# Performance work log

Hardware: AMD Instinct MI355X
Metric: run time of the kernel (lower is better)

The kernel has to match this reference:

```python
import jax, jax.numpy as jnp
import numpy as np

N_HEAD = 16
D_HEAD = 64
D_HIDN = 1024
B, S = 2, 2048
MASK_FILL = -1e9


def setup_inputs() -> dict:
    key = jax.random.key(0)
    ks = jax.random.split(key, 8)
    scale = 1.0 / np.sqrt(D_HIDN)
    return {
        "Q": jax.random.normal(ks[0], (B, S, D_HIDN), dtype=jnp.float32),
        "K": jax.random.normal(ks[1], (B, S, D_HIDN), dtype=jnp.float32),
        "V": jax.random.normal(ks[2], (B, S, D_HIDN), dtype=jnp.float32),
        "attn_mask": jnp.zeros((B, S, S), dtype=jnp.bool_),
        "Wq": jax.random.normal(ks[3], (D_HIDN, N_HEAD * D_HEAD), dtype=jnp.float32) * scale,
        "bq": jnp.zeros((N_HEAD * D_HEAD,), dtype=jnp.float32),
        "Wk": jax.random.normal(ks[4], (D_HIDN, N_HEAD * D_HEAD), dtype=jnp.float32) * scale,
        "bk": jnp.zeros((N_HEAD * D_HEAD,), dtype=jnp.float32),
        "Wv": jax.random.normal(ks[5], (D_HIDN, N_HEAD * D_HEAD), dtype=jnp.float32) * scale,
        "bv": jnp.zeros((N_HEAD * D_HEAD,), dtype=jnp.float32),
        "Wo": jax.random.normal(ks[6], (N_HEAD * D_HEAD, D_HIDN), dtype=jnp.float32) * scale,
        "bo": jnp.zeros((D_HIDN,), dtype=jnp.float32),
    }


def reference(Q, K, V, attn_mask, Wq, bq, Wk, bk, Wv, bv, Wo, bo):
    b, s, _ = Q.shape
    # projections -> [B, H, S, d_head]
    def split_heads(x):
        return x.reshape(b, -1, N_HEAD, D_HEAD).transpose(0, 2, 1, 3)
    q = split_heads(Q @ Wq + bq)
    k = split_heads(K @ Wk + bk)
    v = split_heads(V @ Wv + bv)
    # scaled dot-product attention with masked_fill(-1e9)
    scores = jnp.einsum("bhqd,bhkd->bhqk", q, k) / jnp.sqrt(jnp.float32(D_HEAD))
    scores = jnp.where(attn_mask[:, None, :, :], MASK_FILL, scores)
    attn_prob = jax.nn.softmax(scores, axis=-1)  # [B,H,S,S]
    context = jnp.einsum("bhqk,bhkd->bhqd", attn_prob, v)
    context = context.transpose(0, 2, 1, 3).reshape(b, s, N_HEAD * D_HEAD)
    output = context @ Wo + bo  # dropout is identity at eval
    return output, attn_prob
```

## Files before the change

kernel.cpp:

```cpp
#include <hip/hip_runtime.h>

typedef _Float16 f16;
typedef _Float16 f16x8 __attribute__((ext_vector_type(8)));
typedef _Float16 f16x4v __attribute__((ext_vector_type(4)));
typedef float f32x4 __attribute__((ext_vector_type(4)));

#define B_   2
#define S_   2048
#define H_   16
#define DH   64
#define DM   1024
#define BS_  (B_ * S_)

#if __has_builtin(__builtin_amdgcn_exp2f)
#define EXP2(x) __builtin_amdgcn_exp2f(x)
#else
#define EXP2(x) exp2f(x)
#endif

#define SCHED_FENCE() __builtin_amdgcn_sched_barrier(0)

__device__ __forceinline__ void gload16(const void* g, void* l) {
  __builtin_amdgcn_global_load_lds((const __attribute__((address_space(1))) unsigned int*)g,
                                   (__attribute__((address_space(3))) unsigned int*)l, 16, 0, 0);
}

__global__ __launch_bounds__(256) void prep(const float* __restrict__ Q, const float* __restrict__ K,
                                            const float* __restrict__ V,
                                            f16* __restrict__ Xq, f16* __restrict__ Xk, f16* __restrict__ Xv,
                                            const float* __restrict__ w0, const float* __restrict__ w1,
                                            const float* __restrict__ w2, const float* __restrict__ w3,
                                            f16* __restrict__ t0, f16* __restrict__ t1,
                                            f16* __restrict__ t2, f16* __restrict__ t3,
                                            const unsigned char* __restrict__ mask,
                                            unsigned* __restrict__ mtab) {
  int bid = blockIdx.x;
  int tid = threadIdx.x;
  if (bid < 6144) {
    int t = bid >> 11;
    const float* in = t == 0 ? Q : (t == 1 ? K : V);
    f16* out = t == 0 ? Xq : (t == 1 ? Xk : Xv);
    int i = ((bid & 2047) * 256 + tid) * 8;
    float4 x = *(const float4*)(in + i);
    float4 y = *(const float4*)(in + i + 4);
    f16x8 o;
    o[0] = (f16)x.x; o[1] = (f16)x.y; o[2] = (f16)x.z; o[3] = (f16)x.w;
    o[4] = (f16)y.x; o[5] = (f16)y.y; o[6] = (f16)y.z; o[7] = (f16)y.w;
    *(f16x8*)(out + i) = o;
  } else if (bid < 7168) {
    __shared__ float t[64][65];
    int w = bid - 6144;
    int z = w >> 8, rr = w & 255;
    const float* wsrc = z == 0 ? w0 : (z == 1 ? w1 : (z == 2 ? w2 : w3));
    f16* wt = z == 0 ? t0 : (z == 1 ? t1 : (z == 2 ? t2 : t3));
    int r0 = (rr >> 4) * 64, c0 = (rr & 15) * 64;
    int tr = tid >> 2, seg = tid & 3;
#pragma unroll
    for (int jj = 0; jj < 4; ++jj) {
      float4 v = *(const float4*)(wsrc + (size_t)(r0 + tr) * DM + c0 + seg * 16 + jj * 4);
      t[tr][seg * 16 + jj * 4 + 0] = v.x;
      t[tr][seg * 16 + jj * 4 + 1] = v.y;
      t[tr][seg * 16 + jj * 4 + 2] = v.z;
      t[tr][seg * 16 + jj * 4 + 3] = v.w;
    }
    __syncthreads();
#pragma unroll
    for (int jj = 0; jj < 2; ++jj) {
      f16x8 o;
#pragma unroll
      for (int e = 0; e < 8; ++e) o[e] = (f16)t[seg * 16 + jj * 8 + e][tr];
      *(f16x8*)(wt + (size_t)(c0 + tr) * DM + r0 + seg * 16 + jj * 8) = o;
    }
  } else {
    __shared__ unsigned mbits;
    if (tid == 0) mbits = 0;
    __syncthreads();
    int mb_id = bid - 7168;
    int b = mb_id >> 4, qt = mb_id & 15;
    int row = qt * 128 + (tid >> 1), halfsel = tid & 1;
    const unsigned char* mrow = mask + (size_t)b * S_ * S_ + (size_t)row * S_ + halfsel * 1024;
    unsigned bits = 0;
#pragma unroll
    for (int c = 0; c < 16; ++c) {
      uint4 a0 = *(const uint4*)(mrow + c * 64);
      uint4 a1 = *(const uint4*)(mrow + c * 64 + 16);
      uint4 a2 = *(const uint4*)(mrow + c * 64 + 32);
      uint4 a3 = *(const uint4*)(mrow + c * 64 + 48);
      unsigned z = (a0.x|a0.y|a0.z|a0.w) | (a1.x|a1.y|a1.z|a1.w) |
                   (a2.x|a2.y|a2.z|a2.w) | (a3.x|a3.y|a3.z|a3.w);
      bits |= (z != 0 ? 1u : 0u) << (halfsel * 16 + c);
    }
    if (bits) atomicOr(&mbits, bits);
    __syncthreads();
    if (tid == 0) mtab[mb_id] = mbits;
  }
}

__device__ __forceinline__ void gemm_core(const f16* __restrict__ A,
                                          const f16* __restrict__ Bt,
                                          int m0, int n0,
                                          char (&As)[2][16384], char (&Bs)[2][16384],
                                          f32x4 (&acc)[4][2]) {
  const int tid = threadIdx.x;
  const int lane = tid & 63, wid = tid >> 6;
  const int wr = wid >> 2, wc = wid & 3;
  const int l15 = lane & 15, l4 = lane >> 4;
#pragma unroll
  for (int mi = 0; mi < 4; ++mi)
#pragma unroll
    for (int ni = 0; ni < 2; ++ni) { acc[mi][ni][0]=0.f; acc[mi][ni][1]=0.f; acc[mi][ni][2]=0.f; acc[mi][ni][3]=0.f; }

  auto stage = [&](int buf, int kt) {
#pragma unroll
    for (int j = 0; j < 2; ++j) {
      int L = j * 512 + tid;
      int row = L >> 3, seg = L & 7;
      int so = (seg ^ (row & 7)) << 4;
      gload16((const char*)A + ((size_t)(m0 + row) * DM + kt) * 2 + so,
              As[buf] + j * 8192 + wid * 1024);
      gload16((const char*)Bt + ((size_t)(n0 + row) * DM + kt) * 2 + so,
              Bs[buf] + j * 8192 + wid * 1024);
    }
  };

  stage(0, 0);
  __syncthreads();
  for (int t = 0; t < 16; ++t) {
    int cur = t & 1;
    if (t < 15) stage(cur ^ 1, (t + 1) * 64);
#pragma unroll
    for (int kk = 0; kk < 2; ++kk) {
      f16x8 af[4], bf[2];
#pragma unroll
      for (int mi = 0; mi < 4; ++mi) {
        int row = wr * 64 + mi * 16 + l15;
        af[mi] = *(const f16x8*)(As[cur] + row * 128 + ((kk * 64 + l4 * 16) ^ ((row & 7) << 4)));
      }
#pragma unroll
      for (int ni = 0; ni < 2; ++ni) {
        int row = wc * 32 + ni * 16 + l15;
        bf[ni] = *(const f16x8*)(Bs[cur] + row * 128 + ((kk * 64 + l4 * 16) ^ ((row & 7) << 4)));
      }
#pragma unroll
      for (int mi = 0; mi < 4; ++mi)
#pragma unroll
        for (int ni = 0; ni < 2; ++ni)
          acc[mi][ni] = __builtin_amdgcn_mfma_f32_16x16x32_f16(af[mi], bf[ni], acc[mi][ni], 0, 0, 0);
    }
    __syncthreads();
  }
}

struct GemmPtrs { const f16* A; const f16* Bt; const float* bias; f16* outh; };

__global__ __launch_bounds__(512, 4) void gemm_proj(GemmPtrs p0, GemmPtrs p1, GemmPtrs p2,
                                                    f16* __restrict__ vout) {
  __shared__ __attribute__((aligned(16))) char As[2][16384];
  __shared__ __attribute__((aligned(16))) char Bs[2][16384];
  int lin = (blockIdx.z * 8 + blockIdx.y) * 32 + blockIdx.x;
  int swz = (lin & 7) * 96 + (lin >> 3);
  int z = swz >> 8, r = swz & 255;
  int m0 = (r >> 3) * 128, n0 = (r & 7) * 128;
  GemmPtrs g = z == 0 ? p0 : (z == 1 ? p1 : p2);

  f32x4 acc[4][2];
  gemm_core(g.A, g.Bt, m0, n0, As, Bs, acc);

  const int tid = threadIdx.x;
  const int lane = tid & 63, wid = tid >> 6;
  const int wr = wid >> 2, wc = wid & 3;
  const int l15 = lane & 15, l4 = lane >> 4;

  if (z != 2) {
#pragma unroll
    for (int mi = 0; mi < 4; ++mi)
#pragma unroll
      for (int ni = 0; ni < 2; ++ni) {
        int gcol = n0 + wc * 32 + ni * 16 + l15;
        float bv = g.bias[gcol];
#pragma unroll
        for (int rr = 0; rr < 4; ++rr) {
          int grow = m0 + wr * 64 + mi * 16 + l4 * 4 + rr;
          int b = grow >> 11, s = grow & 2047, h = gcol >> 6, d = gcol & 63;
          g.outh[(size_t)((b * H_ + h) * S_ + s) * DH + d] = (f16)(acc[mi][ni][rr] + bv);
        }
      }
  } else {
    f16* T2 = (f16*)&As[0][0];
    int b = m0 >> 11, s0 = m0 & 2047;
#pragma unroll
    for (int hh = 0; hh < 2; ++hh) {
      if ((wc >> 1) == hh) {
        int dl = (wc & 1) * 32;
#pragma unroll
        for (int mi = 0; mi < 4; ++mi)
#pragma unroll
          for (int ni = 0; ni < 2; ++ni) {
            int d = dl + ni * 16 + l15;
            int sl = wr * 64 + mi * 16 + l4 * 4;
            float bv = g.bias[n0 + hh * 64 + d];
            f16x4v pv;
            pv[0] = (f16)(acc[mi][ni][0] + bv);
            pv[1] = (f16)(acc[mi][ni][1] + bv);
            pv[2] = (f16)(acc[mi][ni][2] + bv);
            pv[3] = (f16)(acc[mi][ni][3] + bv);
            *(f16x4v*)(T2 + d * 136 + sl) = pv;
          }
      }
      __syncthreads();
      {
        int d = tid >> 3, sq = tid & 7;
        int head = (n0 >> 6) + hh;
        const f16* src = T2 + d * 136 + sq * 16;
        f16* dst = vout + ((size_t)((b * H_ + head) * DH + d)) * S_ + s0 + sq * 16;
        *(f16x8*)(dst)     = *(const f16x8*)(src);
        *(f16x8*)(dst + 8) = *(const f16x8*)(src + 8);
      }
      if (hh == 0) __syncthreads();
    }
  }
}

__global__ __launch_bounds__(512, 2) void gemm_out(const f16* __restrict__ A,
                                                   const f16* __restrict__ Bt,
                                                   const float* __restrict__ bias,
                                                   float* __restrict__ outf) {
  __shared__ __attribute__((aligned(16))) char As[2][16384];
  __shared__ __attribute__((aligned(16))) char Bs[2][16384];
  int lin = blockIdx.y * 32 + blockIdx.x;
  int swz = (lin & 7) * 32 + (lin >> 3);
  int m0 = (swz >> 3) * 128, n0 = (swz & 7) * 128;

  f32x4 acc[4][2];
  gemm_core(A, Bt, m0, n0, As, Bs, acc);

  const int tid = threadIdx.x;
  const int lane = tid & 63, wid = tid >> 6;
  const int wr = wid >> 2, wc = wid & 3;
  const int l15 = lane & 15, l4 = lane >> 4;
#pragma unroll
  for (int mi = 0; mi < 4; ++mi)
#pragma unroll
    for (int ni = 0; ni < 2; ++ni) {
      int gcol = n0 + wc * 32 + ni * 16 + l15;
      float bv = bias[gcol];
#pragma unroll
      for (int rr = 0; rr < 4; ++rr) {
        int grow = m0 + wr * 64 + mi * 16 + l4 * 4 + rr;
        outf[(size_t)grow * DM + gcol] = acc[mi][ni][rr] + bv;
      }
    }
}

__global__ __launch_bounds__(512, 4) void attn_kernel(const f16* __restrict__ q,
                                                      const f16* __restrict__ k,
                                                      const f16* __restrict__ vt,
                                                      const unsigned char* __restrict__ mask,
                                                      const unsigned* __restrict__ mtab,
                                                      float* __restrict__ pout,
                                                      f16* __restrict__ ctxh) {
  __shared__ __attribute__((aligned(16))) char KV[4][8192];
  __shared__ __attribute__((aligned(16))) float P32[8][16][68];
  const int tid = threadIdx.x;
  const int lane = tid & 63, wid = tid >> 6;
  const int l15 = lane & 15, l4 = lane >> 4;

  int lin = blockIdx.y * 16 + blockIdx.x;
  int swz = (lin & 7) * 64 + (lin >> 3);
  const int bx = swz & 15, bh = swz >> 4;
  const int b = bh >> 4, h = bh & 15;
  const int q0w = bx * 128 + wid * 16;

  const f16* qb = q + (size_t)bh * S_ * DH;
  const char* kbc = (const char*)(k + (size_t)bh * S_ * DH);
  const char* vtbc = (const char*)(vt + (size_t)bh * DH * S_);
  const unsigned char* mb = mask + (size_t)b * S_ * S_;
  float* pb = pout + (size_t)bh * S_ * S_;

  const int srow = tid >> 3, sseg = tid & 7;
  const int soff = (sseg ^ (srow & 7)) << 4;

  auto stageK = [&](int buf, int t) {
    gload16(kbc + (size_t)(t * 64 + srow) * 128 + soff, KV[buf] + wid * 1024);
  };
  auto stageV = [&](int buf, int t) {
    gload16(vtbc + (size_t)srow * (S_ * 2) + (size_t)(t * 64) * 2 + soff, KV[buf] + wid * 1024);
  };

  const unsigned mmask = mtab[b * 16 + bx];

  const f16 qs = (f16)0.18033688f;
  f16x8 aq[2];
#pragma unroll
  for (int hh = 0; hh < 2; ++hh) {
    f16x8 v = *(const f16x8*)(qb + (size_t)(q0w + l15) * DH + hh * 32 + l4 * 8);
#pragma unroll
    for (int j = 0; j < 8; ++j) v[j] = v[j] * qs;
    aq[hh] = v;
  }
  SCHED_FENCE();

  float sm[4] = {0.f, 0.f, 0.f, 0.f};

  stageK(0, 0);
  stageK(1, 1);
  for (int p = 0; p < 16; ++p) {
    asm volatile("s_waitcnt vmcnt(0)" ::: "memory");
    __builtin_amdgcn_s_barrier();
    SCHED_FENCE();
    if (p < 15) { stageK((2 * p + 2) & 3, 2 * p + 2); stageK((2 * p + 3) & 3, 2 * p + 3); }
    SCHED_FENCE();
#pragma unroll
    for (int u = 0; u < 2; ++u) {
      const int t = 2 * p + u;
      const char* Kb = KV[t & 3];
      const int kt = t * 64;
      const int anym = (mmask >> t) & 1;
#pragma unroll
      for (int f = 0; f < 4; ++f) {
        int krow = f * 16 + l15;
        f16x8 bk0 = *(const f16x8*)(Kb + krow * 128 + ((l4 * 16) ^ ((krow & 7) << 4)));
        f16x8 bk1 = *(const f16x8*)(Kb + krow * 128 + ((64 + l4 * 16) ^ ((krow & 7) << 4)));
        f32x4 s; s[0]=0.f; s[1]=0.f; s[2]=0.f; s[3]=0.f;
        __builtin_amdgcn_s_setprio(1);
        s = __builtin_amdgcn_mfma_f32_16x16x32_f16(aq[0], bk0, s, 0, 0, 0);
        s = __builtin_amdgcn_mfma_f32_16x16x32_f16(aq[1], bk1, s, 0, 0, 0);
        __builtin_amdgcn_s_setprio(0);
#pragma unroll
        for (int rr = 0; rr < 4; ++rr) {
          float sv = s[rr];
          if (anym) sv = mb[(size_t)(q0w + l4 * 4 + rr) * S_ + kt + f * 16 + l15] ? -1e9f : sv;
          sm[rr] += EXP2(sv);
        }
      }
    }
  }
#pragma unroll
  for (int d = 1; d < 16; d <<= 1)
#pragma unroll
    for (int rr = 0; rr < 4; ++rr) sm[rr] += __shfl_xor(sm[rr], d);
  float inv[4];
#pragma unroll
  for (int rr = 0; rr < 4; ++rr) inv[rr] = 1.0f / sm[rr];

  f32x4 ctx[4];
#pragma unroll
  for (int dc = 0; dc < 4; ++dc) { ctx[dc][0]=0.f; ctx[dc][1]=0.f; ctx[dc][2]=0.f; ctx[dc][3]=0.f; }

  __builtin_amdgcn_s_barrier();
  stageK(0, 0);
  stageV(2, 0);
  __syncthreads();
  for (int t = 0; t < 32; ++t) {
    const int cur = t & 1;
    const int kt = t * 64;
    if (t < 31) { stageK(cur ^ 1, t + 1); stageV(2 + (cur ^ 1), t + 1); }
    SCHED_FENCE();
    const int anym = (mmask >> t) & 1;

#pragma unroll
    for (int f = 0; f < 4; ++f) {
      int krow = f * 16 + l15;
      f16x8 bk0 = *(const f16x8*)(KV[cur] + krow * 128 + ((l4 * 16) ^ ((krow & 7) << 4)));
      f16x8 bk1 = *(const f16x8*)(KV[cur] + krow * 128 + ((64 + l4 * 16) ^ ((krow & 7) << 4)));
      f32x4 s; s[0]=0.f; s[1]=0.f; s[2]=0.f; s[3]=0.f;
      __builtin_amdgcn_s_setprio(1);
      s = __builtin_amdgcn_mfma_f32_16x16x32_f16(aq[0], bk0, s, 0, 0, 0);
      s = __builtin_amdgcn_mfma_f32_16x16x32_f16(aq[1], bk1, s, 0, 0, 0);
      __builtin_amdgcn_s_setprio(0);
#pragma unroll
      for (int rr = 0; rr < 4; ++rr) {
        float sv = s[rr];
        if (anym) sv = mb[(size_t)(q0w + l4 * 4 + rr) * S_ + kt + f * 16 + l15] ? -1e9f : sv;
        float p = EXP2(sv) * inv[rr];
        P32[wid][l4 * 4 + rr][f * 16 + l15] = p;
      }
    }
#pragma unroll
    for (int j = 0; j < 4; ++j) {
      int row = j * 4 + l4;
      f32x4 v = *(const f32x4*)&P32[wid][row][l15 * 4];
      __builtin_nontemporal_store(v, (f32x4*)(pb + (size_t)(q0w + row) * S_ + kt + l15 * 4));
    }
#pragma unroll
    for (int kk = 0; kk < 2; ++kk) {
      f32x4 x = *(const f32x4*)&P32[wid][l15][kk * 32 + l4 * 8];
      f32x4 y = *(const f32x4*)&P32[wid][l15][kk * 32 + l4 * 8 + 4];
      f16x8 pa;
      pa[0] = (f16)x[0]; pa[1] = (f16)x[1]; pa[2] = (f16)x[2]; pa[3] = (f16)x[3];
      pa[4] = (f16)y[0]; pa[5] = (f16)y[1]; pa[6] = (f16)y[2]; pa[7] = (f16)y[3];
      f16x8 bv0, bv1, bv2, bv3;
      {
        int vr0 = 0 * 16 + l15, vr1 = 1 * 16 + l15, vr2 = 2 * 16 + l15, vr3 = 3 * 16 + l15;
        bv0 = *(const f16x8*)(KV[2 + cur] + vr0 * 128 + ((kk * 64 + l4 * 16) ^ ((vr0 & 7) << 4)));
        bv1 = *(const f16x8*)(KV[2 + cur] + vr1 * 128 + ((kk * 64 + l4 * 16) ^ ((vr1 & 7) << 4)));
        bv2 = *(const f16x8*)(KV[2 + cur] + vr2 * 128 + ((kk * 64 + l4 * 16) ^ ((vr2 & 7) << 4)));
        bv3 = *(const f16x8*)(KV[2 + cur] + vr3 * 128 + ((kk * 64 + l4 * 16) ^ ((vr3 & 7) << 4)));
      }
      __builtin_amdgcn_s_setprio(1);
      ctx[0] = __builtin_amdgcn_mfma_f32_16x16x32_f16(pa, bv0, ctx[0], 0, 0, 0);
      ctx[1] = __builtin_amdgcn_mfma_f32_16x16x32_f16(pa, bv1, ctx[1], 0, 0, 0);
      ctx[2] = __builtin_amdgcn_mfma_f32_16x16x32_f16(pa, bv2, ctx[2], 0, 0, 0);
      ctx[3] = __builtin_amdgcn_mfma_f32_16x16x32_f16(pa, bv3, ctx[3], 0, 0, 0);
      __builtin_amdgcn_s_setprio(0);
    }

    if (t < 31) {
      asm volatile("s_waitcnt vmcnt(4)" ::: "memory");
      __builtin_amdgcn_s_barrier();
      SCHED_FENCE();
    }
  }

  {
    f16* cst = (f16*)&P32[wid][0][0];
#pragma unroll
    for (int dc = 0; dc < 4; ++dc)
#pragma unroll
      for (int rr = 0; rr < 4; ++rr)
        cst[(l4 * 4 + rr) * 72 + dc * 16 + l15] = (f16)ctx[dc][rr];
#pragma unroll
    for (int j = 0; j < 4; ++j) {
      int row = j * 4 + l4;
      f16x4v v = *(const f16x4v*)(cst + row * 72 + l15 * 4);
      *(f16x4v*)(ctxh + (size_t)(b * S_ + q0w + row) * DM + h * DH + l15 * 4) = v;
    }
  }
}

extern "C" void kernel_launch(void* const* d_in, const int* in_sizes, int n_in,
                              void* d_out, int out_size, void* d_ws, size_t ws_size,
                              hipStream_t stream) {
  (void)in_sizes; (void)n_in; (void)out_size; (void)ws_size;
  const float* Q  = (const float*)d_in[0];
  const float* K  = (const float*)d_in[1];
  const float* V  = (const float*)d_in[2];
  const unsigned char* mask = (const unsigned char*)d_in[3];
  const float* Wq = (const float*)d_in[4];
  const float* bq = (const float*)d_in[5];
  const float* Wk = (const float*)d_in[6];
  const float* bk = (const float*)d_in[7];
  const float* Wv = (const float*)d_in[8];
  const float* bv = (const float*)d_in[9];
  const float* Wo = (const float*)d_in[10];
  const float* bo = (const float*)d_in[11];

  f16* ws = (f16*)d_ws;
  f16* Xq  = ws;
  f16* Xk  = Xq + 4194304;
  f16* Xv  = Xk + 4194304;
  f16* Wqt = Xv + 4194304;
  f16* Wkt = Wqt + 1048576;
  f16* Wvt = Wkt + 1048576;
  f16* Wot = Wvt + 1048576;
  f16* qh  = Wot + 1048576;
  f16* kh  = qh + 4194304;
  f16* vth = kh + 4194304;
  unsigned* mtab = (unsigned*)(vth + 4194304);
  f16* ctx = Xq;

  float* out0 = (float*)d_out;
  float* pout = out0 + (size_t)BS_ * DM;

  prep<<<dim3(7200), dim3(256), 0, stream>>>(Q, K, V, Xq, Xk, Xv,
                                             Wq, Wk, Wv, Wo, Wqt, Wkt, Wvt, Wot,
                                             mask, mtab);

  GemmPtrs pq{Xq, Wqt, bq, qh};
  GemmPtrs pk{Xk, Wkt, bk, kh};
  GemmPtrs pv{Xv, Wvt, bv, nullptr};
  gemm_proj<<<dim3(32, 8, 3), dim3(512), 0, stream>>>(pq, pk, pv, vth);

  attn_kernel<<<dim3(16, 32), dim3(512), 0, stream>>>(qh, kh, vth, mask, mtab, pout, ctx);

  gemm_out<<<dim3(32, 8), dim3(512), 0, stream>>>(ctx, Wot, bo, out0);
}
```

Measured before the change: 228.1 us.

## Fuse fp32-to-fp16 activation conversion into projection GEMM A-tile loading

Drops the separate conversion of Q/K/V to fp16 from the prep kernel. The projection GEMM now loads fp32 A tiles straight into registers, converts them, and writes them into swizzled LDS after the MFMA step, overlapping with compute. This removes a full write and re-read of 24MB of fp16 activations. In exchange the A loads now go through registers, which raises register pressure in a kernel launched with a 4-blocks occupancy bound, and A traffic into the GEMM doubles because fp32 is read.

```diff
diff --git a/kernel.cpp b/kernel.cpp
--- a/kernel.cpp
+++ b/kernel.cpp
@@ -25,10 +25,7 @@
                                    (__attribute__((address_space(3))) unsigned int*)l, 16, 0, 0);
 }
 
-__global__ __launch_bounds__(256) void prep(const float* __restrict__ Q, const float* __restrict__ K,
-                                            const float* __restrict__ V,
-                                            f16* __restrict__ Xq, f16* __restrict__ Xk, f16* __restrict__ Xv,
-                                            const float* __restrict__ w0, const float* __restrict__ w1,
+__global__ __launch_bounds__(256) void prep(const float* __restrict__ w0, const float* __restrict__ w1,
                                             const float* __restrict__ w2, const float* __restrict__ w3,
                                             f16* __restrict__ t0, f16* __restrict__ t1,
                                             f16* __restrict__ t2, f16* __restrict__ t3,
@@ -36,21 +33,9 @@
                                             unsigned* __restrict__ mtab) {
   int bid = blockIdx.x;
   int tid = threadIdx.x;
-  if (bid < 6144) {
-    int t = bid >> 11;
-    const float* in = t == 0 ? Q : (t == 1 ? K : V);
-    f16* out = t == 0 ? Xq : (t == 1 ? Xk : Xv);
-    int i = ((bid & 2047) * 256 + tid) * 8;
-    float4 x = *(const float4*)(in + i);
-    float4 y = *(const float4*)(in + i + 4);
-    f16x8 o;
-    o[0] = (f16)x.x; o[1] = (f16)x.y; o[2] = (f16)x.z; o[3] = (f16)x.w;
-    o[4] = (f16)y.x; o[5] = (f16)y.y; o[6] = (f16)y.z; o[7] = (f16)y.w;
-    *(f16x8*)(out + i) = o;
-  } else if (bid < 7168) {
+  if (bid < 1024) {
     __shared__ float t[64][65];
-    int w = bid - 6144;
-    int z = w >> 8, rr = w & 255;
+    int z = bid >> 8, rr = bid & 255;
     const float* wsrc = z == 0 ? w0 : (z == 1 ? w1 : (z == 2 ? w2 : w3));
     f16* wt = z == 0 ? t0 : (z == 1 ? t1 : (z == 2 ? t2 : t3));
     int r0 = (rr >> 4) * 64, c0 = (rr & 15) * 64;
@@ -75,7 +60,7 @@
     __shared__ unsigned mbits;
     if (tid == 0) mbits = 0;
     __syncthreads();
-    int mb_id = bid - 7168;
+    int mb_id = bid - 1024;
     int b = mb_id >> 4, qt = mb_id & 15;
     int row = qt * 128 + (tid >> 1), halfsel = tid & 1;
     const unsigned char* mrow = mask + (size_t)b * S_ * S_ + (size_t)row * S_ + halfsel * 1024;
@@ -96,7 +81,8 @@
   }
 }
 
-__device__ __forceinline__ void gemm_core(const f16* __restrict__ A,
+template <bool A32>
+__device__ __forceinline__ void gemm_core(const void* __restrict__ Ap,
                                           const f16* __restrict__ Bt,
                                           int m0, int n0,
                                           char (&As)[2][16384], char (&Bs)[2][16384],
@@ -110,24 +96,76 @@
 #pragma unroll
     for (int ni = 0; ni < 2; ++ni) { acc[mi][ni][0]=0.f; acc[mi][ni][1]=0.f; acc[mi][ni][2]=0.f; acc[mi][ni][3]=0.f; }
 
-  auto stage = [&](int buf, int kt) {
+  const int arow = tid >> 2, aquad = tid & 3;
+  const float* Af = (const float*)Ap;
+  const f16* Ah = (const f16*)Ap;
+
+  f32x4 areg[4];
+  auto issueA = [&](int kt) {
+    if (A32) {
+#pragma unroll
+      for (int u = 0; u < 4; ++u)
+        areg[u] = *(const f32x4*)(Af + (size_t)(m0 + arow) * DM + kt + aquad * 16 + u * 4);
+    } else {
+#pragma unroll
+      for (int j = 0; j < 2; ++j) {
+        int L = j * 512 + tid;
+        int row = L >> 3, seg = L & 7;
+        int so = (seg ^ (row & 7)) << 4;
+        gload16((const char*)Ah + ((size_t)(m0 + row) * DM + 0) * 2 + (size_t)kt * 2 + so,
+                As[0] + j * 8192 + wid * 1024);
+      }
+    }
+  };
+  (void)issueA;
+
+  auto stageB = [&](int buf, int kt) {
 #pragma unroll
     for (int j = 0; j < 2; ++j) {
       int L = j * 512 + tid;
       int row = L >> 3, seg = L & 7;
       int so = (seg ^ (row & 7)) << 4;
-      gload16((const char*)A + ((size_t)(m0 + row) * DM + kt) * 2 + so,
-              As[buf] + j * 8192 + wid * 1024);
       gload16((const char*)Bt + ((size_t)(n0 + row) * DM + kt) * 2 + so,
               Bs[buf] + j * 8192 + wid * 1024);
     }
   };
-
-  stage(0, 0);
+  auto stageA16 = [&](int buf, int kt) {
+#pragma unroll
+    for (int j = 0; j < 2; ++j) {
+      int L = j * 512 + tid;
+      int row = L >> 3, seg = L & 7;
+      int so = (seg ^ (row & 7)) << 4;
+      gload16((const char*)Ah + ((size_t)(m0 + row) * DM + kt) * 2 + so,
+              As[buf] + j * 8192 + wid * 1024);
+    }
+  };
+  auto loadA32 = [&](int kt) {
+#pragma unroll
+    for (int u = 0; u < 4; ++u)
+      areg[u] = *(const f32x4*)(Af + (size_t)(m0 + arow) * DM + kt + aquad * 16 + u * 4);
+  };
+  auto writeA32 = [&](int buf) {
+    f16x8 h0, h1;
+#pragma unroll
+    for (int j = 0; j < 4; ++j) { h0[j] = (f16)areg[0][j]; h0[4 + j] = (f16)areg[1][j]; }
+#pragma unroll
+    for (int j = 0; j < 4; ++j) { h1[j] = (f16)areg[2][j]; h1[4 + j] = (f16)areg[3][j]; }
+    int swz = (arow & 7) << 4;
+    *(f16x8*)(As[buf] + arow * 128 + ((aquad * 32) ^ swz)) = h0;
+    *(f16x8*)(As[buf] + arow * 128 + ((aquad * 32 + 16) ^ swz)) = h1;
+  };
+
+  if (A32) { loadA32(0); writeA32(0); } else { stageA16(0, 0); }
+  stageB(0, 0);
   __syncthreads();
+
   for (int t = 0; t < 16; ++t) {
     int cur = t & 1;
-    if (t < 15) stage(cur ^ 1, (t + 1) * 64);
+    if (t < 15) {
+      if (A32) loadA32((t + 1) * 64);
+      else stageA16(cur ^ 1, (t + 1) * 64);
+      stageB(cur ^ 1, (t + 1) * 64);
+    }
 #pragma unroll
     for (int kk = 0; kk < 2; ++kk) {
       f16x8 af[4], bf[2];
@@ -147,11 +185,12 @@
         for (int ni = 0; ni < 2; ++ni)
           acc[mi][ni] = __builtin_amdgcn_mfma_f32_16x16x32_f16(af[mi], bf[ni], acc[mi][ni], 0, 0, 0);
     }
+    if (A32 && t < 15) writeA32(cur ^ 1);
     __syncthreads();
   }
 }
 
-struct GemmPtrs { const f16* A; const f16* Bt; const float* bias; f16* outh; };
+struct GemmPtrs { const float* A; const f16* Bt; const float* bias; f16* outh; };
 
 __global__ __launch_bounds__(512, 4) void gemm_proj(GemmPtrs p0, GemmPtrs p1, GemmPtrs p2,
                                                     f16* __restrict__ vout) {
@@ -164,7 +203,7 @@
   GemmPtrs g = z == 0 ? p0 : (z == 1 ? p1 : p2);
 
   f32x4 acc[4][2];
-  gemm_core(g.A, g.Bt, m0, n0, As, Bs, acc);
+  gemm_core<true>(g.A, g.Bt, m0, n0, As, Bs, acc);
 
   const int tid = threadIdx.x;
   const int lane = tid & 63, wid = tid >> 6;
@@ -232,7 +271,7 @@
   int m0 = (swz >> 3) * 128, n0 = (swz & 7) * 128;
 
   f32x4 acc[4][2];
-  gemm_core(A, Bt, m0, n0, As, Bs, acc);
+  gemm_core<false>(A, Bt, m0, n0, As, Bs, acc);
 
   const int tid = threadIdx.x;
   const int lane = tid & 63, wid = tid >> 6;
@@ -446,10 +485,8 @@
   const float* bo = (const float*)d_in[11];
 
   f16* ws = (f16*)d_ws;
-  f16* Xq  = ws;
-  f16* Xk  = Xq + 4194304;
-  f16* Xv  = Xk + 4194304;
-  f16* Wqt = Xv + 4194304;
+  f16* ctx = ws;
+  f16* Wqt = ctx + 4194304;
   f16* Wkt = Wqt + 1048576;
   f16* Wvt = Wkt + 1048576;
   f16* Wot = Wvt + 1048576;
@@ -457,18 +494,16 @@
   f16* kh  = qh + 4194304;
   f16* vth = kh + 4194304;
   unsigned* mtab = (unsigned*)(vth + 4194304);
-  f16* ctx = Xq;
 
   float* out0 = (float*)d_out;
   float* pout = out0 + (size_t)BS_ * DM;
 
-  prep<<<dim3(7200), dim3(256), 0, stream>>>(Q, K, V, Xq, Xk, Xv,
-                                             Wq, Wk, Wv, Wo, Wqt, Wkt, Wvt, Wot,
+  prep<<<dim3(1056), dim3(256), 0, stream>>>(Wq, Wk, Wv, Wo, Wqt, Wkt, Wvt, Wot,
                                              mask, mtab);
 
-  GemmPtrs pq{Xq, Wqt, bq, qh};
-  GemmPtrs pk{Xk, Wkt, bk, kh};
-  GemmPtrs pv{Xv, Wvt, bv, nullptr};
+  GemmPtrs pq{Q, Wqt, bq, qh};
+  GemmPtrs pk{K, Wkt, bk, kh};
+  GemmPtrs pv{V, Wvt, bv, nullptr};
   gemm_proj<<<dim3(32, 8, 3), dim3(512), 0, stream>>>(pq, pk, pv, vth);
 
   attn_kernel<<<dim3(16, 32), dim3(512), 0, stream>>>(qh, kh, vth, mask, mtab, pout, ctx);
```

New measurement: 238.3 us. +4.5%, slower.
